# Performance work log

Hardware: AMD Instinct MI355X
Metric: run time of the kernel (lower is better)

## Reference

```python
import jax, jax.numpy as jnp
import numpy as np

TEMPERATURE = 1.0

def setup_inputs() -> dict:
    key = jax.random.key(0)
    k1, k2 = jax.random.split(key)
    B, I, O = 256, 1024, 1024
    x = jax.random.normal(k1, (B, I), dtype=jnp.float32)
    # mimic TruncatedNormal(stddev=1/sqrt(input_size)) init
    w = jax.random.normal(k2, (I, O), dtype=jnp.float32) * (1.0 / np.sqrt(I))
    b = jnp.zeros((O,), dtype=jnp.float32)
    return {"x": x, "w": w, "b": b}

def reference(x, w, b):
    # z: [B, I, O] outer product per sample
    z = jnp.einsum('bi,io->bio', x, w)
    n = x.shape[-1]
    # per-output-neuron temperature softmax over the input dim I
    s = jax.nn.softmax(jnp.abs(z) / TEMPERATURE, axis=1)
    out = n * jnp.sum(z * s, axis=1)  # [B, O]
    return out + b
```

## Files before the change

kernel.cpp:

```cpp
#include <hip/hip_runtime.h>

#define BDIM 256
#define IDIM 1024
#define ODIM 1024

#define NW 8
#define TILE_OL 2
#define TILE_O (64 * TILE_OL)
#define TILE_B 2
#define QLEN (IDIM / NW)
#define CHUNK 8
#define NCHUNK (QLEN / CHUNK)

typedef float v2f __attribute__((ext_vector_type(2)));
typedef float v4f __attribute__((ext_vector_type(4)));

#if __has_builtin(__builtin_amdgcn_exp2f)
#define FAST_EXP2(v) __builtin_amdgcn_exp2f(v)
#else
#define FAST_EXP2(v) exp2f(v)
#endif

__global__ __launch_bounds__(512, 6)
void stl_kernel(const float* __restrict__ x,
                const float* __restrict__ w,
                const float* __restrict__ bias,
                float* __restrict__ out) {
  __shared__ float xs[TILE_B][IDIM];
  __shared__ float ps[NW][64][8];

  const int tx = threadIdx.x;
  const int ty = threadIdx.y;
  const int tid = ty * 64 + tx;
  const int o0 = blockIdx.x * TILE_O;
  const int b0 = blockIdx.y * TILE_B;

  const float LOG2E = 1.4426950408889634f;

  {
    int row = tid >> 8;
    int col = tid & 255;
    float4 v = ((const float4*)(x + (size_t)(b0 + row) * IDIM))[col];
    v.x *= LOG2E; v.y *= LOG2E; v.z *= LOG2E; v.w *= LOG2E;
    ((float4*)(&xs[row][0]))[col] = v;
  }
  __syncthreads();

  const int qbase = ty * QLEN;
  const float* wp = w + (size_t)qbase * ODIM + o0 + tx;

  v2f an[TILE_OL][TILE_B], ad[TILE_OL][TILE_B];
#pragma unroll
  for (int s = 0; s < TILE_OL; ++s)
#pragma unroll
    for (int r = 0; r < TILE_B; ++r) { an[s][r] = (v2f){0.f, 0.f}; ad[s][r] = (v2f){0.f, 0.f}; }

  v2f wA0[CHUNK / 2], wA1[CHUNK / 2], wB0[CHUNK / 2], wB1[CHUNK / 2];

#define WLOADF(d0_, d1_, cc)                                              \
  {                                                                       \
    const float* wq = wp + (size_t)((cc) * CHUNK) * ODIM;                 \
    _Pragma("unroll")                                                     \
    for (int u = 0; u < CHUNK / 2; ++u) {                                 \
      d0_[u].x = wq[(size_t)(2 * u) * ODIM];                              \
      d0_[u].y = wq[(size_t)(2 * u + 1) * ODIM];                          \
      d1_[u].x = wq[(size_t)(2 * u) * ODIM + 64];                         \
      d1_[u].y = wq[(size_t)(2 * u + 1) * ODIM + 64];                     \
    }                                                                     \
  }

#define ROWPF(acc_n, acc_d, xpair, wpair)                                 \
  {                                                                       \
    v2f p = (xpair) * (wpair);                \
    v2f t;                                                                \
    t.x = FAST_EXP2(__builtin_fabsf(p.x));     \
    t.y = FAST_EXP2(__builtin_fabsf(p.y));                                \
    acc_n += p * t;                                         \
    acc_d += t;                                             \
  }

#define LOF(xq) __builtin_shufflevector(xq, xq, 0, 1)
#define HIF(xq) __builtin_shufflevector(xq, xq, 2, 3)

#define COMPUTEF(wc0, wc1, cc)                                            \
  {                                                                       \
    const int jb = qbase + (cc) * CHUNK;                                  \
    _Pragma("unroll")                                                     \
    for (int h = 0; h < 2; ++h) {                                         \
      v4f xq[TILE_B];                                                     \
      _Pragma("unroll")                                                   \
      for (int r = 0; r < TILE_B; ++r)                                    \
        xq[r] = *(const v4f*)(&xs[r][jb + h * 4]);                        \
      _Pragma("unroll")                                                   \
      for (int r = 0; r < TILE_B; ++r) {                                  \
        ROWPF(an[0][r], ad[0][r], LOF(xq[r]), wc0[h * 2])                 \
        ROWPF(an[0][r], ad[0][r], HIF(xq[r]), wc0[h * 2 + 1])             \
        ROWPF(an[1][r], ad[1][r], LOF(xq[r]), wc1[h * 2])                 \
        ROWPF(an[1][r], ad[1][r], HIF(xq[r]), wc1[h * 2 + 1])             \
      }                                                                   \
    }                                                                     \
  }

  WLOADF(wA0, wA1, 0)
  for (int c = 0; c < NCHUNK; c += 2) {
    WLOADF(wB0, wB1, c + 1)
    COMPUTEF(wA0, wA1, c)
    WLOADF(wA0, wA1, (c + 2) & (NCHUNK - 1))
    COMPUTEF(wB0, wB1, c + 1)
  }

  *(float4*)(&ps[ty][tx][0]) =
      make_float4(an[0][0].x + an[0][0].y, an[0][1].x + an[0][1].y,
                  an[1][0].x + an[1][0].y, an[1][1].x + an[1][1].y);
  *(float4*)(&ps[ty][tx][4]) =
      make_float4(ad[0][0].x + ad[0][0].y, ad[0][1].x + ad[0][1].y,
                  ad[1][0].x + ad[1][0].y, ad[1][1].x + ad[1][1].y);
  __syncthreads();

  if (tid < 256) {
    const int txp = tid & 63;
    const int s = (tid >> 6) & 1;
    const int bq = tid >> 7;
    float n = 0.f, d = 0.f;
#pragma unroll
    for (int wv = 0; wv < NW; ++wv) {
      n += ps[wv][txp][s * 2 + bq];
      d += ps[wv][txp][4 + s * 2 + bq];
    }
    const float LN2 = 0.6931471805599453f;
    const float scale = (float)IDIM * LN2;
    const int o = o0 + s * 64 + txp;
    out[(size_t)(b0 + bq) * ODIM + o] = scale * n / d + bias[o];
  }
}

extern "C" void kernel_launch(void* const* d_in, const int* in_sizes, int n_in,
                              void* d_out, int out_size, void* d_ws, size_t ws_size,
                              hipStream_t stream) {
  const float* x = (const float*)d_in[0];
  const float* w = (const float*)d_in[1];
  const float* b = (const float*)d_in[2];
  float* out = (float*)d_out;

  dim3 grid(ODIM / TILE_O, BDIM / TILE_B);
  dim3 block(64, NW);
  stl_kernel<<<grid, block, 0, stream>>>(x, w, b, out);
}
```

Measured before the change: 94.67 us.

## Widen output tile to four columns per thread with vectorized float4 weight loads

Each thread now covers four adjacent output columns, loaded as one float4 per weight row instead of scalar loads strided by 64, which doubles the block's output tile to 256 columns and halves the number of blocks along O. The chunk depth is halved to keep the register count for prefetched weights roughly the same, and the occupancy hint drops from 6 to 4 blocks. The final reduction layout in shared memory is reorganized and padded to match the new per-thread column mapping, and all 512 threads now take part in it. The aim is fewer, wider global load instructions and better reuse of each x value. The cost is higher register pressure, lower occupancy and half as many blocks to fill the device.

Measured after the change: 94.17 us. No clear change (-0.5%).

```diff
diff --git a/kernel.cpp b/kernel.cpp
--- a/kernel.cpp
+++ b/kernel.cpp
@@ -5,11 +5,11 @@
 #define ODIM 1024
 
 #define NW 8
-#define TILE_OL 2
-#define TILE_O (64 * TILE_OL)
+#define OL 4
+#define TILE_O (64 * OL)
 #define TILE_B 2
 #define QLEN (IDIM / NW)
-#define CHUNK 8
+#define CHUNK 4
 #define NCHUNK (QLEN / CHUNK)
 
 typedef float v2f __attribute__((ext_vector_type(2)));
@@ -21,13 +21,13 @@
 #define FAST_EXP2(v) exp2f(v)
 #endif
 
-__global__ __launch_bounds__(512, 6)
+__global__ __launch_bounds__(512, 4)
 void stl_kernel(const float* __restrict__ x,
                 const float* __restrict__ w,
                 const float* __restrict__ bias,
                 float* __restrict__ out) {
   __shared__ float xs[TILE_B][IDIM];
-  __shared__ float ps[NW][64][8];
+  __shared__ float ps[NW][16][68];
 
   const int tx = threadIdx.x;
   const int ty = threadIdx.y;
@@ -47,89 +47,94 @@
   __syncthreads();
 
   const int qbase = ty * QLEN;
-  const float* wp = w + (size_t)qbase * ODIM + o0 + tx;
+  const float* wp = w + (size_t)qbase * ODIM + o0 + 4 * tx;
 
-  v2f an[TILE_OL][TILE_B], ad[TILE_OL][TILE_B];
+  v2f an[2][TILE_B], ad[2][TILE_B];
 #pragma unroll
-  for (int s = 0; s < TILE_OL; ++s)
+  for (int s = 0; s < 2; ++s)
 #pragma unroll
     for (int r = 0; r < TILE_B; ++r) { an[s][r] = (v2f){0.f, 0.f}; ad[s][r] = (v2f){0.f, 0.f}; }
 
-  v2f wA0[CHUNK / 2], wA1[CHUNK / 2], wB0[CHUNK / 2], wB1[CHUNK / 2];
+  v4f wA[CHUNK], wB[CHUNK];
 
-#define WLOADF(d0_, d1_, cc)                                              \
+#define WLOADQ(dst, cc)                                                   \
   {                                                                       \
     const float* wq = wp + (size_t)((cc) * CHUNK) * ODIM;                 \
     _Pragma("unroll")                                                     \
-    for (int u = 0; u < CHUNK / 2; ++u) {                                 \
-      d0_[u].x = wq[(size_t)(2 * u) * ODIM];                              \
-      d0_[u].y = wq[(size_t)(2 * u + 1) * ODIM];                          \
-      d1_[u].x = wq[(size_t)(2 * u) * ODIM + 64];                         \
-      d1_[u].y = wq[(size_t)(2 * u + 1) * ODIM + 64];                     \
-    }                                                                     \
+    for (int u = 0; u < CHUNK; ++u)                                       \
+      dst[u] = *(const v4f*)(wq + (size_t)u * ODIM);                      \
   }
 
-#define ROWPF(acc_n, acc_d, xpair, wpair)                                 \
+#define ROWPQ(acc_n, acc_d, xx, wpair)                                    \
   {                                                                       \
-    v2f p = (xpair) * (wpair);                \
+    v2f p = (xx) * (wpair);                   \
     v2f t;                                                                \
-    t.x = FAST_EXP2(__builtin_fabsf(p.x));     \
+    t.x = FAST_EXP2(__builtin_fabsf(p.x));                                \
     t.y = FAST_EXP2(__builtin_fabsf(p.y));                                \
     acc_n += p * t;                                         \
     acc_d += t;                                             \
   }
 
-#define LOF(xq) __builtin_shufflevector(xq, xq, 0, 1)
-#define HIF(xq) __builtin_shufflevector(xq, xq, 2, 3)
+#define LOQ(q) __builtin_shufflevector(q, q, 0, 1)
+#define HIQ(q) __builtin_shufflevector(q, q, 2, 3)
 
-#define COMPUTEF(wc0, wc1, cc)                                            \
+#define STEPQ(wc, xq0, xq1, ii)                                           \
+  {                                                                       \
+    v2f wlo = LOQ(wc[ii]), whi = HIQ(wc[ii]);                             \
+    v2f x0 = __builtin_shufflevector(xq0, xq0, ii, ii);                   \
+    v2f x1 = __builtin_shufflevector(xq1, xq1, ii, ii);                   \
+    ROWPQ(an[0][0], ad[0][0], x0, wlo)                                    \
+    ROWPQ(an[1][0], ad[1][0], x0, whi)                                    \
+    ROWPQ(an[0][1], ad[0][1], x1, wlo)                                    \
+    ROWPQ(an[1][1], ad[1][1], x1, whi)                                    \
+  }
+
+#define COMPUTEQ(wc, cc)                                                  \
   {                                                                       \
     const int jb = qbase + (cc) * CHUNK;                                  \
-    _Pragma("unroll")                                                     \
-    for (int h = 0; h < 2; ++h) {                                         \
-      v4f xq[TILE_B];                                                     \
-      _Pragma("unroll")                                                   \
-      for (int r = 0; r < TILE_B; ++r)                                    \
-        xq[r] = *(const v4f*)(&xs[r][jb + h * 4]);                        \
-      _Pragma("unroll")                                                   \
-      for (int r = 0; r < TILE_B; ++r) {                                  \
-        ROWPF(an[0][r], ad[0][r], LOF(xq[r]), wc0[h * 2])                 \
-        ROWPF(an[0][r], ad[0][r], HIF(xq[r]), wc0[h * 2 + 1])             \
-        ROWPF(an[1][r], ad[1][r], LOF(xq[r]), wc1[h * 2])                 \
-        ROWPF(an[1][r], ad[1][r], HIF(xq[r]), wc1[h * 2 + 1])             \
-      }                                                                   \
-    }                                                                     \
+    v4f xq0 = *(const v4f*)(&xs[0][jb]);      \
+    v4f xq1 = *(const v4f*)(&xs[1][jb]);                                  \
+    STEPQ(wc, xq0, xq1, 0)                                                \
+    STEPQ(wc, xq0, xq1, 1)                                                \
+    STEPQ(wc, xq0, xq1, 2)                                                \
+    STEPQ(wc, xq0, xq1, 3)                                                \
   }
 
-  WLOADF(wA0, wA1, 0)
+  WLOADQ(wA, 0)
   for (int c = 0; c < NCHUNK; c += 2) {
-    WLOADF(wB0, wB1, c + 1)
-    COMPUTEF(wA0, wA1, c)
-    WLOADF(wA0, wA1, (c + 2) & (NCHUNK - 1))
-    COMPUTEF(wB0, wB1, c + 1)
+    WLOADQ(wB, c + 1)
+    COMPUTEQ(wA, c)
+    WLOADQ(wA, (c + 2) & (NCHUNK - 1))
+    COMPUTEQ(wB, c + 1)
   }
 
-  *(float4*)(&ps[ty][tx][0]) =
-      make_float4(an[0][0].x + an[0][0].y, an[0][1].x + an[0][1].y,
-                  an[1][0].x + an[1][0].y, an[1][1].x + an[1][1].y);
-  *(float4*)(&ps[ty][tx][4]) =
-      make_float4(ad[0][0].x + ad[0][0].y, ad[0][1].x + ad[0][1].y,
-                  ad[1][0].x + ad[1][0].y, ad[1][1].x + ad[1][1].y);
+#pragma unroll
+  for (int bq = 0; bq < TILE_B; ++bq) {
+    ps[ty][bq * 8 + 0][tx] = an[0][bq].x;
+    ps[ty][bq * 8 + 1][tx] = an[0][bq].y;
+    ps[ty][bq * 8 + 2][tx] = an[1][bq].x;
+    ps[ty][bq * 8 + 3][tx] = an[1][bq].y;
+    ps[ty][bq * 8 + 4][tx] = ad[0][bq].x;
+    ps[ty][bq * 8 + 5][tx] = ad[0][bq].y;
+    ps[ty][bq * 8 + 6][tx] = ad[1][bq].x;
+    ps[ty][bq * 8 + 7][tx] = ad[1][bq].y;
+  }
   __syncthreads();
 
-  if (tid < 256) {
-    const int txp = tid & 63;
-    const int s = (tid >> 6) & 1;
-    const int bq = tid >> 7;
+  {
+    const int o_rel = tid & 255;
+    const int bq = tid >> 8;
+    const int t = o_rel >> 2;
+    const int k = o_rel & 3;
     float n = 0.f, d = 0.f;
 #pragma unroll
     for (int wv = 0; wv < NW; ++wv) {
-      n += ps[wv][txp][s * 2 + bq];
-      d += ps[wv][txp][4 + s * 2 + bq];
+      n += ps[wv][bq * 8 + k][t];
+      d += ps[wv][bq * 8 + 4 + k][t];
     }
     const float LN2 = 0.6931471805599453f;
     const float scale = (float)IDIM * LN2;
-    const int o = o0 + s * 64 + txp;
+    const int o = o0 + o_rel;
     out[(size_t)(b0 + bq) * ODIM + o] = scale * n / d + bias[o];
   }
 }
```
